# Optimization experiments

Hardware: AMD Instinct MI355X
Metric: run time of the kernel (lower is better)

Reference implementation:

```python
import jax, jax.numpy as jnp
import numpy as np

DIMS = [64, 128, 192, 256]   # Matryoshka sub-dims (init arg `dims`)
TEMPERATURE = 1.0
NEG_INF = float('-inf')
EPS = 1e-12  # F.normalize eps


def setup_inputs() -> dict:
    key = jax.random.key(0)
    k1, k2 = jax.random.split(key)
    B, K, D = 2048, 4096, 256
    reps_q = jax.random.normal(k1, (B, D), dtype=jnp.float32)
    reps_d = jax.random.normal(k2, (K, D), dtype=jnp.float32)
    return {"reps_q": reps_q, "reps_d": reps_d}


def _l2_normalize(x):
    n = jnp.linalg.norm(x, axis=1, keepdims=True)
    return x / jnp.maximum(n, EPS)


def _loss_for_dim(reps_q, reps_d, dim):
    q = _l2_normalize(reps_q[:, :dim])   # [B, dim]
    d = _l2_normalize(reps_d[:, :dim])   # [K, dim]
    B, K = q.shape[0], d.shape[0]

    qk = q @ d.T                         # [B, K]

    # check_pos_neg_pair_conflict (always True in the torch code)
    pos = d[:B]                          # positives are the first B keys
    sim = jax.lax.stop_gradient(pos @ d.T)               # [B, K], detached
    eye_bk = jnp.eye(B, K, dtype=bool)
    conflict = jnp.isclose(sim, 1.0, rtol=1e-5, atol=1e-5) & ~eye_bk
    qk = jnp.where(conflict, NEG_INF, qk)

    # use_all_pairs=True path: kq, qq, kk with -inf diagonals
    eye_bb = jnp.eye(B, dtype=bool)
    kq = jnp.where(eye_bb, NEG_INF, pos @ q.T)           # [B, B]
    qq = jnp.where(eye_bb, NEG_INF, q @ q.T)             # [B, B]
    kk = jnp.where(eye_bb, NEG_INF, pos @ pos.T)         # [B, B]

    scores = jnp.concatenate([qk, kq, qq, kk], axis=1)   # [B, K+3B]

    # check_false_neg: mask entries above diag(scores)+0.1 (thresholds detached)
    # diag(scores)[i] = scores[i, i] = qk[i, i] since B <= K
    thr = jax.lax.stop_gradient(jnp.diagonal(qk))[:, None] + 0.1
    scores = jnp.where(scores > thr, NEG_INF, scores)

    # cross-entropy with labels = arange(B)
    logp = jax.nn.log_softmax(scores / TEMPERATURE, axis=1)
    idx = jnp.arange(B)
    return -jnp.mean(logp[idx, idx])


def reference(reps_q, reps_d):
    loss = 0.0
    for dim in DIMS:
        loss = loss + _loss_for_dim(reps_q, reps_d, dim)
    return loss / len(DIMS)
```

## Files before the change

kernel.cpp:

```cpp
#include <hip/hip_runtime.h>

#define B_N 2048
#define K_N 4096
#define D_N 256
#define GRID_SCORE 3072
#define LOG2E 1.44269504f

typedef unsigned short u16;
typedef unsigned int u32;
typedef short short8 __attribute__((ext_vector_type(8)));
typedef float f32x4 __attribute__((ext_vector_type(4)));

__device__ __forceinline__ u16 f2bf(float x) {
    union { float f; u32 u; } v; v.f = x;
    u32 u = v.u;
    u32 lsb = (u >> 16) & 1u;
    u += 0x7fffu + lsb;
    return (u16)(u >> 16);
}
__device__ __forceinline__ float bits2f(u32 u) {
    union { u32 u; float f; } v; v.u = u; return v.f;
}

__global__ __launch_bounds__(256) void prep_kernel(
    const float* __restrict__ qsrc, const float* __restrict__ dsrc,
    u16* __restrict__ qb, u16* __restrict__ db,
    float* __restrict__ invnq, float* __restrict__ invnd, float* __restrict__ diag,
    float* __restrict__ rowsum, u32* __restrict__ doneCnt)
{
    if (blockIdx.x < 32) rowsum[blockIdx.x * 256 + threadIdx.x] = 0.f;
    if (blockIdx.x == 32 && threadIdx.x == 0)
        __hip_atomic_store(doneCnt, 0u, __ATOMIC_RELAXED, __HIP_MEMORY_SCOPE_AGENT);

    const int wave = threadIdx.x >> 6;
    const int lane = threadIdx.x & 63;
    const int row  = blockIdx.x * 4 + wave;

    if (row < B_N) {
        const int i = row;
        float4 qv = *(const float4*)(qsrc + i * D_N + lane * 4);
        float4 dv = *(const float4*)(dsrc + i * D_N + lane * 4);
        ushort4 qs; qs.x = f2bf(qv.x); qs.y = f2bf(qv.y); qs.z = f2bf(qv.z); qs.w = f2bf(qv.w);
        *(ushort4*)(qb + i * D_N + lane * 4) = qs;
        float sqq = qv.x*qv.x + qv.y*qv.y + qv.z*qv.z + qv.w*qv.w;
        float sdd = dv.x*dv.x + dv.y*dv.y + dv.z*dv.z + dv.w*dv.w;
        float sqd = qv.x*dv.x + qv.y*dv.y + qv.z*dv.z + qv.w*dv.w;
        #pragma unroll
        for (int m = 1; m < 16; m <<= 1) {
            sqq += __shfl_xor(sqq, m);
            sdd += __shfl_xor(sdd, m);
            sqd += __shfl_xor(sqd, m);
        }
        float gq0 = __shfl(sqq, 0),  gq1 = __shfl(sqq, 16), gq2 = __shfl(sqq, 32), gq3 = __shfl(sqq, 48);
        float gd0 = __shfl(sdd, 0),  gd1 = __shfl(sdd, 16), gd2 = __shfl(sdd, 32), gd3 = __shfl(sdd, 48);
        float gp0 = __shfl(sqd, 0),  gp1 = __shfl(sqd, 16), gp2 = __shfl(sqd, 32), gp3 = __shfl(sqd, 48);
        if (lane < 4) {
            float pq = gq0, pd = gd0, pp = gp0;
            if (lane >= 1) { pq += gq1; pd += gd1; pp += gp1; }
            if (lane >= 2) { pq += gq2; pd += gd2; pp += gp2; }
            if (lane >= 3) { pq += gq3; pd += gd3; pp += gp3; }
            float inq = 1.0f / fmaxf(sqrtf(pq), 1e-12f);
            float ind = 1.0f / fmaxf(sqrtf(pd), 1e-12f);
            invnq[i * 4 + lane] = inq;
            diag[i * 4 + lane]  = pp * inq * ind;
        }
    } else {
        const int j = row - B_N;
        float4 dv = *(const float4*)(dsrc + j * D_N + lane * 4);
        ushort4 ds; ds.x = f2bf(dv.x); ds.y = f2bf(dv.y); ds.z = f2bf(dv.z); ds.w = f2bf(dv.w);
        *(ushort4*)(db + j * D_N + lane * 4) = ds;
        float sdd = dv.x*dv.x + dv.y*dv.y + dv.z*dv.z + dv.w*dv.w;
        #pragma unroll
        for (int m = 1; m < 16; m <<= 1) sdd += __shfl_xor(sdd, m);
        float gd0 = __shfl(sdd, 0), gd1 = __shfl(sdd, 16), gd2 = __shfl(sdd, 32), gd3 = __shfl(sdd, 48);
        if (lane < 4) {
            float pd = gd0;
            if (lane >= 1) pd += gd1;
            if (lane >= 2) pd += gd2;
            if (lane >= 3) pd += gd3;
            invnd[j * 4 + lane] = 1.0f / fmaxf(sqrtf(pd), 1e-12f);
        }
    }
}

template<int RGN, bool EYE>
__device__ __forceinline__ void epi_seg(
    const f32x4* accq, const f32x4* accd,
    const float* ldsInvAq, const float* ldsInvAd, const float* ldsThr,
    const float* ldsInvB, float* ldsAcc,
    int s, int wrow, int quad, int lane15)
{
    const int myr = wrow + quad * 4;
    f32x4 ivAq = *(const f32x4*)(ldsInvAq + s * 64 + myr);
    f32x4 ivAd = *(const f32x4*)(ldsInvAd + s * 64 + myr);
    f32x4 thrv = *(const f32x4*)(ldsThr   + s * 64 + myr);
    float rsd[4] = {0.f, 0.f, 0.f, 0.f};
    #pragma unroll
    for (int ct = 0; ct < 4; ++ct) {
        const float ivB = ldsInvB[s * 64 + ct * 16 + lane15];
        const int jloc = ct * 16 + lane15;
        #pragma unroll
        for (int r = 0; r < 4; ++r) {
            const float thr = thrv[r];
            const float sq = accq[ct][r] * (ivAq[r] * ivB);
            const float sd = accd[ct][r] * (ivAd[r] * ivB);
            const bool eye = EYE && ((myr + r) == jloc);
            float add = 0.f;
            if (RGN <= 1) {
                bool conflict = (fabsf(sd - LOG2E) <= 2e-5f * LOG2E);
                if (EYE) conflict = conflict && !eye;
                if (!conflict && sq <= thr) add += exp2f(sq);
                if (RGN == 0) {
                    bool okk = (sd <= thr);
                    if (EYE) okk = okk && !eye;
                    if (okk) add += exp2f(sd);
                }
            } else {
                bool o1 = (sd <= thr), o2 = (sq <= thr);
                if (EYE) { o1 = o1 && !eye; o2 = o2 && !eye; }
                if (o1) add += exp2f(sd);
                if (o2) add += exp2f(sq);
            }
            rsd[r] += add;
        }
    }
    #pragma unroll
    for (int r = 0; r < 4; ++r) {
        float v = rsd[r];
        v += __shfl_xor(v, 1);
        v += __shfl_xor(v, 2);
        v += __shfl_xor(v, 4);
        v += __shfl_xor(v, 8);
        if (lane15 == 0)
            ldsAcc[(myr + r) * 4 + s] += v;
    }
}

#define LSB 264
__global__ __launch_bounds__(256, 4) void score_kernel(
    const u16* __restrict__ qb, const u16* __restrict__ db,
    const float* __restrict__ invnq, const float* __restrict__ invnd,
    const float* __restrict__ diag, float* __restrict__ rowsum,
    u32* __restrict__ doneCnt, u32* __restrict__ out)
{
    __shared__ u16   ldsB[64 * LSB];
    __shared__ float ldsInvAq[4 * 64];
    __shared__ float ldsInvAd[4 * 64];
    __shared__ float ldsThr[4 * 64];
    __shared__ float ldsInvB[4 * 64];
    __shared__ float ldsAcc[256];
    __shared__ u32   ldsLast;

    const int cb = blockIdx.x % 96;
    const int rb = blockIdx.x / 96;
    const int IR = rb * 64;
    const int JC = cb * 64;
    const bool isR3 = (cb >= 64);
    const bool isR1 = (cb < 32);
    const u16*  bsrc     = isR3 ? qb : db;
    const float* invBsrc = isR3 ? invnq : invnd;
    const int JB = isR3 ? (JC - K_N) : JC;
    const int sel = isR1 ? ((cb == rb) ? 1 : 0)
                  : (!isR3 ? 2 : (((cb - 64) == rb) ? 4 : 3));

    const int tid    = threadIdx.x;
    const int lane   = tid & 63;
    const int lane15 = lane & 15;
    const int quad   = lane >> 4;
    const int wrow   = (tid >> 6) * 16;

    {
        const int row = tid >> 2, s = tid & 3;
        ldsInvAq[s * 64 + row] = invnq[(IR + row) * 4 + s] * LOG2E;
        ldsInvAd[s * 64 + row] = invnd[(IR + row) * 4 + s] * LOG2E;
        ldsThr[s * 64 + row]   = (diag[(IR + row) * 4 + s] + 0.1f) * LOG2E;
        ldsInvB[s * 64 + row]  = invBsrc[(JB + row) * 4 + s];
        ldsAcc[tid] = 0.f;
    }

    #pragma unroll
    for (int c = 0; c < 8; ++c) {
        int idx = tid + c * 256;
        int row = idx >> 5;
        int ch  = idx & 31;
        uint4 v = *(const uint4*)(bsrc + (JB + row) * D_N + ch * 8);
        *(uint4*)(ldsB + row * LSB + ch * 8) = v;
    }

    const u16* qrowp = qb + (IR + wrow + lane15) * D_N + quad * 8;
    const u16* drowp = db + (IR + wrow + lane15) * D_N + quad * 8;

    short8 aq0 = *(const short8*)(qrowp);
    short8 aq1 = *(const short8*)(qrowp + 32);
    short8 ad0 = *(const short8*)(drowp);
    short8 ad1 = *(const short8*)(drowp + 32);

    __syncthreads();

    f32x4 accq[4], accd[4];
    #pragma unroll
    for (int ct = 0; ct < 4; ++ct) {
        accq[ct] = (f32x4){0.f, 0.f, 0.f, 0.f};
        accd[ct] = (f32x4){0.f, 0.f, 0.f, 0.f};
    }

    #pragma clang loop unroll(disable)
    for (int s = 0; s < 4; ++s) {
        const int sn = ((s + 1) & 3) * 64;
        short8 nq0 = *(const short8*)(qrowp + sn);
        short8 nq1 = *(const short8*)(qrowp + sn + 32);
        short8 nd0 = *(const short8*)(drowp + sn);
        short8 nd1 = *(const short8*)(drowp + sn + 32);

        #pragma unroll
        for (int ct = 0; ct < 4; ++ct) {
            short8 b0 = *(const short8*)(ldsB + (ct * 16 + lane15) * LSB + s * 64 + quad * 8);
            accq[ct] = __builtin_amdgcn_mfma_f32_16x16x32_bf16(aq0, b0, accq[ct], 0, 0, 0);
            accd[ct] = __builtin_amdgcn_mfma_f32_16x16x32_bf16(ad0, b0, accd[ct], 0, 0, 0);
        }
        #pragma unroll
        for (int ct = 0; ct < 4; ++ct) {
            short8 b1 = *(const short8*)(ldsB + (ct * 16 + lane15) * LSB + s * 64 + 32 + quad * 8);
            accq[ct] = __builtin_amdgcn_mfma_f32_16x16x32_bf16(aq1, b1, accq[ct], 0, 0, 0);
            accd[ct] = __builtin_amdgcn_mfma_f32_16x16x32_bf16(ad1, b1, accd[ct], 0, 0, 0);
        }
        if (sel == 0)      epi_seg<0,false>(accq, accd, ldsInvAq, ldsInvAd, ldsThr, ldsInvB, ldsAcc, s, wrow, quad, lane15);
        else if (sel == 1) epi_seg<0,true >(accq, accd, ldsInvAq, ldsInvAd, ldsThr, ldsInvB, ldsAcc, s, wrow, quad, lane15);
        else if (sel == 2) epi_seg<1,false>(accq, accd, ldsInvAq, ldsInvAd, ldsThr, ldsInvB, ldsAcc, s, wrow, quad, lane15);
        else if (sel == 3) epi_seg<2,false>(accq, accd, ldsInvAq, ldsInvAd, ldsThr, ldsInvB, ldsAcc, s, wrow, quad, lane15);
        else               epi_seg<2,true >(accq, accd, ldsInvAq, ldsInvAd, ldsThr, ldsInvB, ldsAcc, s, wrow, quad, lane15);

        aq0 = nq0; aq1 = nq1; ad0 = nd0; ad1 = nd1;
    }
    __syncthreads();

    atomicAdd(&rowsum[IR * 4 + tid], ldsAcc[tid]);
    __syncthreads();
    if (tid == 0) {
        u32 tk = __hip_atomic_fetch_add(doneCnt, 1u, __ATOMIC_RELAXED,
                                        __HIP_MEMORY_SCOPE_AGENT);
        ldsLast = (tk == (GRID_SCORE - 1)) ? 1u : 0u;
    }
    __syncthreads();

    if (ldsLast) {
        float acc = 0.f;
        #pragma unroll 8
        for (int c = 0; c < 32; ++c) {
            int idx = tid + c * 256;
            float rsv = __hip_atomic_load(&rowsum[idx], __ATOMIC_RELAXED,
                                          __HIP_MEMORY_SCOPE_AGENT);
            acc += logf(rsv) - diag[idx];
        }
        ldsAcc[tid] = acc;
        __syncthreads();
        #pragma unroll
        for (int off = 128; off > 0; off >>= 1) {
            if (tid < off) ldsAcc[tid] += ldsAcc[tid + off];
            __syncthreads();
        }
        if (tid == 0) {
            float L = ldsAcc[0] * (1.0f / (B_N * 4.0f));
            u16 h = f2bf(L);
            union { float f; u32 u; } b; b.f = L;
            u32 c0 = (b.u & 0xFFFF0000u) | (u32)h;
            u32 c1 = c0 + 0x10000u;
            u32 c2 = c0 - 0x10000u;
            float e0 = fabsf(bits2f(c0) - L);
            float e1 = fabsf(bits2f(c1) - L);
            float e2 = fabsf(bits2f(c2) - L);
            u32 best = c0; float be = e0;
            if (e1 < be) { best = c1; be = e1; }
            if (e2 < be) { best = c2; }
            out[0] = best;
        }
    }
}

extern "C" void kernel_launch(void* const* d_in, const int* in_sizes, int n_in,
                              void* d_out, int out_size, void* d_ws, size_t ws_size,
                              hipStream_t stream) {
    (void)in_sizes; (void)n_in; (void)out_size; (void)ws_size;
    const float* qsrc = (const float*)d_in[0];
    const float* dsrc = (const float*)d_in[1];
    char* ws = (char*)d_ws;
    u16*   qb      = (u16*)ws;
    u16*   db      = (u16*)(ws + 1048576);
    float* invnq   = (float*)(ws + 3145728);
    float* invnd   = (float*)(ws + 3178496);
    float* diag    = (float*)(ws + 3244032);
    float* rowsum  = (float*)(ws + 3276800);
    u32*   doneCnt = (u32*)(ws + 3309568);

    prep_kernel<<<1536, 256, 0, stream>>>(qsrc, dsrc, qb, db, invnq, invnd, diag,
                                          rowsum, doneCnt);
    score_kernel<<<GRID_SCORE, 256, 0, stream>>>(qb, db, invnq, invnd, diag, rowsum,
                                                 doneCnt, (u32*)d_out);
}
```

Measured before the change: 112.5 us.

## Exploit transpose symmetry of score blocks to skip redundant tile computations

The kq block is the transpose of the leading qk block, and qq is symmetric. Tiles are therefore restructured into four modes: qk+kk tiles that also add column contributions for kq, plain qk tiles, diagonal qq tiles, and upper-triangular qq tiles that add both row and column sums. This cuts the grid from 3072 to 2576 blocks and removes one MFMA stream from the q-only tiles. In exchange it adds LDS atomics for the column partials, extra global atomics into rowsum, and a small serial loop per block to decode the triangular index.

New measurement: 117.0 us. +4.0%, slower.

```diff
diff --git a/kernel.cpp b/kernel.cpp
--- a/kernel.cpp
+++ b/kernel.cpp
@@ -3,7 +3,7 @@
 #define B_N 2048
 #define K_N 4096
 #define D_N 256
-#define GRID_SCORE 3072
+#define GRID_SCORE 2576
 #define LOG2E 1.44269504f
 
 typedef unsigned short u16;
@@ -83,11 +83,11 @@
     }
 }
 
-template<int RGN, bool EYE>
-__device__ __forceinline__ void epi_seg(
+template<bool KK, bool EYE>
+__device__ __forceinline__ void epi2(
     const f32x4* accq, const f32x4* accd,
     const float* ldsInvAq, const float* ldsInvAd, const float* ldsThr,
-    const float* ldsInvB, float* ldsAcc,
+    const float* ldsInvB, const float* ldsThrB, float* ldsAcc, float* ldsAccCol,
     int s, int wrow, int quad, int lane15)
 {
     const int myr = wrow + quad * 4;
@@ -97,31 +97,79 @@
     float rsd[4] = {0.f, 0.f, 0.f, 0.f};
     #pragma unroll
     for (int ct = 0; ct < 4; ++ct) {
-        const float ivB = ldsInvB[s * 64 + ct * 16 + lane15];
         const int jloc = ct * 16 + lane15;
+        const float ivB  = ldsInvB[s * 64 + jloc];
+        const float thrB = KK ? ldsThrB[s * 64 + jloc] : 0.f;
+        float colp = 0.f;
         #pragma unroll
         for (int r = 0; r < 4; ++r) {
-            const float thr = thrv[r];
             const float sq = accq[ct][r] * (ivAq[r] * ivB);
             const float sd = accd[ct][r] * (ivAd[r] * ivB);
             const bool eye = EYE && ((myr + r) == jloc);
-            float add = 0.f;
-            if (RGN <= 1) {
-                bool conflict = (fabsf(sd - LOG2E) <= 2e-5f * LOG2E);
-                if (EYE) conflict = conflict && !eye;
-                if (!conflict && sq <= thr) add += exp2f(sq);
-                if (RGN == 0) {
-                    bool okk = (sd <= thr);
-                    if (EYE) okk = okk && !eye;
-                    if (okk) add += exp2f(sd);
-                }
+            bool conflict = (fabsf(sd - LOG2E) <= 2e-5f * LOG2E);
+            if (EYE) conflict = conflict && !eye;
+            const float eq = exp2f(sq);
+            if (!conflict && sq <= thrv[r]) rsd[r] += eq;
+            if (KK) {
+                bool okk = (sd <= thrv[r]);
+                if (EYE) okk = okk && !eye;
+                if (okk) rsd[r] += exp2f(sd);
+                bool okq = (sq <= thrB);
+                if (EYE) okq = okq && !eye;
+                if (okq) colp += eq;
+            }
+        }
+        if (KK) {
+            colp += __shfl_xor(colp, 16);
+            colp += __shfl_xor(colp, 32);
+            if (quad == 0) atomicAdd(&ldsAccCol[jloc * 4 + s], colp);
+        }
+    }
+    #pragma unroll
+    for (int r = 0; r < 4; ++r) {
+        float v = rsd[r];
+        v += __shfl_xor(v, 1);
+        v += __shfl_xor(v, 2);
+        v += __shfl_xor(v, 4);
+        v += __shfl_xor(v, 8);
+        if (lane15 == 0)
+            ldsAcc[(myr + r) * 4 + s] += v;
+    }
+}
+
+template<bool DUAL>
+__device__ __forceinline__ void epiQ(
+    const f32x4* accq,
+    const float* ldsInvAq, const float* ldsThr,
+    const float* ldsInvB, const float* ldsThrB, float* ldsAcc, float* ldsAccCol,
+    int s, int wrow, int quad, int lane15)
+{
+    const int myr = wrow + quad * 4;
+    f32x4 ivAq = *(const f32x4*)(ldsInvAq + s * 64 + myr);
+    f32x4 thrv = *(const f32x4*)(ldsThr   + s * 64 + myr);
+    float rsd[4] = {0.f, 0.f, 0.f, 0.f};
+    #pragma unroll
+    for (int ct = 0; ct < 4; ++ct) {
+        const int jloc = ct * 16 + lane15;
+        const float ivB  = ldsInvB[s * 64 + jloc];
+        const float thrB = DUAL ? ldsThrB[s * 64 + jloc] : 0.f;
+        float colp = 0.f;
+        #pragma unroll
+        for (int r = 0; r < 4; ++r) {
+            const float sq = accq[ct][r] * (ivAq[r] * ivB);
+            const float e = exp2f(sq);
+            if (!DUAL) {
+                const bool eye = ((myr + r) == jloc);
+                if (!eye && sq <= thrv[r]) rsd[r] += e;
             } else {
-                bool o1 = (sd <= thr), o2 = (sq <= thr);
-                if (EYE) { o1 = o1 && !eye; o2 = o2 && !eye; }
-                if (o1) add += exp2f(sd);
-                if (o2) add += exp2f(sq);
-            }
-            rsd[r] += add;
+                if (sq <= thrv[r]) rsd[r] += e;
+                if (sq <= thrB)    colp  += e;
+            }
+        }
+        if (DUAL) {
+            colp += __shfl_xor(colp, 16);
+            colp += __shfl_xor(colp, 32);
+            if (quad == 0) atomicAdd(&ldsAccCol[jloc * 4 + s], colp);
         }
     }
     #pragma unroll
@@ -148,20 +196,27 @@
     __shared__ float ldsInvAd[4 * 64];
     __shared__ float ldsThr[4 * 64];
     __shared__ float ldsInvB[4 * 64];
+    __shared__ float ldsThrB[4 * 64];
     __shared__ float ldsAcc[256];
-    __shared__ u32   ldsLast;
-
-    const int cb = blockIdx.x % 96;
-    const int rb = blockIdx.x / 96;
+    __shared__ float ldsAccCol[256];
+
+    const int bid = blockIdx.x;
+    int rb, cbl, mode;
+    if (bid < 1024)      { mode = 0; rb = bid >> 5; cbl = bid & 31; }
+    else if (bid < 2048) { mode = 1; int b = bid - 1024; rb = b >> 5; cbl = b & 31; }
+    else if (bid < 2080) { mode = 2; rb = bid - 2048; cbl = rb; }
+    else {
+        mode = 3; int k = bid - 2080; int a = 0;
+        while (k >= 31 - a) { k -= 31 - a; ++a; }
+        rb = a; cbl = a + 1 + k;
+    }
+    const bool qpl  = (mode >= 2);
+    const bool col  = (mode == 0 || mode == 3);
+    const bool eyeB = (mode == 0 && rb == cbl);
     const int IR = rb * 64;
-    const int JC = cb * 64;
-    const bool isR3 = (cb >= 64);
-    const bool isR1 = (cb < 32);
-    const u16*  bsrc     = isR3 ? qb : db;
-    const float* invBsrc = isR3 ? invnq : invnd;
-    const int JB = isR3 ? (JC - K_N) : JC;
-    const int sel = isR1 ? ((cb == rb) ? 1 : 0)
-                  : (!isR3 ? 2 : (((cb - 64) == rb) ? 4 : 3));
+    const int JB = (mode == 1) ? (B_N + cbl * 64) : (cbl * 64);
+    const u16*  bsrc     = qpl ? qb : db;
+    const float* invBsrc = qpl ? invnq : invnd;
 
     const int tid    = threadIdx.x;
     const int lane   = tid & 63;
@@ -175,7 +230,9 @@
         ldsInvAd[s * 64 + row] = invnd[(IR + row) * 4 + s] * LOG2E;
         ldsThr[s * 64 + row]   = (diag[(IR + row) * 4 + s] + 0.1f) * LOG2E;
         ldsInvB[s * 64 + row]  = invBsrc[(JB + row) * 4 + s];
+        ldsThrB[s * 64 + row]  = col ? (diag[(JB + row) * 4 + s] + 0.1f) * LOG2E : 0.f;
         ldsAcc[tid] = 0.f;
+        ldsAccCol[tid] = 0.f;
     }
 
     #pragma unroll
@@ -190,60 +247,87 @@
     const u16* qrowp = qb + (IR + wrow + lane15) * D_N + quad * 8;
     const u16* drowp = db + (IR + wrow + lane15) * D_N + quad * 8;
 
-    short8 aq0 = *(const short8*)(qrowp);
-    short8 aq1 = *(const short8*)(qrowp + 32);
-    short8 ad0 = *(const short8*)(drowp);
-    short8 ad1 = *(const short8*)(drowp + 32);
-
+    if (!qpl) {
+        short8 aq0 = *(const short8*)(qrowp);
+        short8 aq1 = *(const short8*)(qrowp + 32);
+        short8 ad0 = *(const short8*)(drowp);
+        short8 ad1 = *(const short8*)(drowp + 32);
+        __syncthreads();
+
+        f32x4 accq[4], accd[4];
+        #pragma unroll
+        for (int ct = 0; ct < 4; ++ct) {
+            accq[ct] = (f32x4){0.f, 0.f, 0.f, 0.f};
+            accd[ct] = (f32x4){0.f, 0.f, 0.f, 0.f};
+        }
+        #pragma clang loop unroll(disable)
+        for (int s = 0; s < 4; ++s) {
+            const int sn = ((s + 1) & 3) * 64;
+            short8 nq0 = *(const short8*)(qrowp + sn);
+            short8 nq1 = *(const short8*)(qrowp + sn + 32);
+            short8 nd0 = *(const short8*)(drowp + sn);
+            short8 nd1 = *(const short8*)(drowp + sn + 32);
+            #pragma unroll
+            for (int ct = 0; ct < 4; ++ct) {
+                short8 b0 = *(const short8*)(ldsB + (ct * 16 + lane15) * LSB + s * 64 + quad * 8);
+                accq[ct] = __builtin_amdgcn_mfma_f32_16x16x32_bf16(aq0, b0, accq[ct], 0, 0, 0);
+                accd[ct] = __builtin_amdgcn_mfma_f32_16x16x32_bf16(ad0, b0, accd[ct], 0, 0, 0);
+            }
+            #pragma unroll
+            for (int ct = 0; ct < 4; ++ct) {
+                short8 b1 = *(const short8*)(ldsB + (ct * 16 + lane15) * LSB + s * 64 + 32 + quad * 8);
+                accq[ct] = __builtin_amdgcn_mfma_f32_16x16x32_bf16(aq1, b1, accq[ct], 0, 0, 0);
+                accd[ct] = __builtin_amdgcn_mfma_f32_16x16x32_bf16(ad1, b1, accd[ct], 0, 0, 0);
+            }
+            if (mode == 0) {
+                if (eyeB) epi2<true,true >(accq, accd, ldsInvAq, ldsInvAd, ldsThr, ldsInvB, ldsThrB, ldsAcc, ldsAccCol, s, wrow, quad, lane15);
+                else      epi2<true,false>(accq, accd, ldsInvAq, ldsInvAd, ldsThr, ldsInvB, ldsThrB, ldsAcc, ldsAccCol, s, wrow, quad, lane15);
+            } else {
+                epi2<false,false>(accq, accd, ldsInvAq, ldsInvAd, ldsThr, ldsInvB, ldsThrB, ldsAcc, ldsAccCol, s, wrow, quad, lane15);
+            }
+            aq0 = nq0; aq1 = nq1; ad0 = nd0; ad1 = nd1;
+        }
+    } else {
+        short8 aq0 = *(const short8*)(qrowp);
+        short8 aq1 = *(const short8*)(qrowp + 32);
+        __syncthreads();
+
+        f32x4 accq[4];
+        #pragma unroll
+        for (int ct = 0; ct < 4; ++ct) accq[ct] = (f32x4){0.f, 0.f, 0.f, 0.f};
+        #pragma clang loop unroll(disable)
+        for (int s = 0; s < 4; ++s) {
+            const int sn = ((s + 1) & 3) * 64;
+            short8 nq0 = *(const short8*)(qrowp + sn);
+            short8 nq1 = *(const short8*)(qrowp + sn + 32);
+            #pragma unroll
+            for (int ct = 0; ct < 4; ++ct) {
+                short8 b0 = *(const short8*)(ldsB + (ct * 16 + lane15) * LSB + s * 64 + quad * 8);
+                accq[ct] = __builtin_amdgcn_mfma_f32_16x16x32_bf16(aq0, b0, accq[ct], 0, 0, 0);
+            }
+            #pragma unroll
+            for (int ct = 0; ct < 4; ++ct) {
+                short8 b1 = *(const short8*)(ldsB + (ct * 16 + lane15) * LSB + s * 64 + 32 + quad * 8);
+                accq[ct] = __builtin_amdgcn_mfma_f32_16x16x32_bf16(aq1, b1, accq[ct], 0, 0, 0);
+            }
+            if (mode == 2) epiQ<false>(accq, ldsInvAq, ldsThr, ldsInvB, ldsThrB, ldsAcc, ldsAccCol, s, wrow, quad, lane15);
+            else           epiQ<true >(accq, ldsInvAq, ldsThr, ldsInvB, ldsThrB, ldsAcc, ldsAccCol, s, wrow, quad, lane15);
+            aq0 = nq0; aq1 = nq1;
+        }
+    }
     __syncthreads();
 
-    f32x4 accq[4], accd[4];
-    #pragma unroll
-    for (int ct = 0; ct < 4; ++ct) {
-        accq[ct] = (f32x4){0.f, 0.f, 0.f, 0.f};
-        accd[ct] = (f32x4){0.f, 0.f, 0.f, 0.f};
-    }
-
-    #pragma clang loop unroll(disable)
-    for (int s = 0; s < 4; ++s) {
-        const int sn = ((s + 1) & 3) * 64;
-        short8 nq0 = *(const short8*)(qrowp + sn);
-        short8 nq1 = *(const short8*)(qrowp + sn + 32);
-        short8 nd0 = *(const short8*)(drowp + sn);
-        short8 nd1 = *(const short8*)(drowp + sn + 32);
-
-        #pragma unroll
-        for (int ct = 0; ct < 4; ++ct) {
-            short8 b0 = *(const short8*)(ldsB + (ct * 16 + lane15) * LSB + s * 64 + quad * 8);
-            accq[ct] = __builtin_amdgcn_mfma_f32_16x16x32_bf16(aq0, b0, accq[ct], 0, 0, 0);
-            accd[ct] = __builtin_amdgcn_mfma_f32_16x16x32_bf16(ad0, b0, accd[ct], 0, 0, 0);
-        }
-        #pragma unroll
-        for (int ct = 0; ct < 4; ++ct) {
-            short8 b1 = *(const short8*)(ldsB + (ct * 16 + lane15) * LSB + s * 64 + 32 + quad * 8);
-            accq[ct] = __builtin_amdgcn_mfma_f32_16x16x32_bf16(aq1, b1, accq[ct], 0, 0, 0);
-            accd[ct] = __builtin_amdgcn_mfma_f32_16x16x32_bf16(ad1, b1, accd[ct], 0, 0, 0);
-        }
-        if (sel == 0)      epi_seg<0,false>(accq, accd, ldsInvAq, ldsInvAd, ldsThr, ldsInvB, ldsAcc, s, wrow, quad, lane15);
-        else if (sel == 1) epi_seg<0,true >(accq, accd, ldsInvAq, ldsInvAd, ldsThr, ldsInvB, ldsAcc, s, wrow, quad, lane15);
-        else if (sel == 2) epi_seg<1,false>(accq, accd, ldsInvAq, ldsInvAd, ldsThr, ldsInvB, ldsAcc, s, wrow, quad, lane15);
-        else if (sel == 3) epi_seg<2,false>(accq, accd, ldsInvAq, ldsInvAd, ldsThr, ldsInvB, ldsAcc, s, wrow, quad, lane15);
-        else               epi_seg<2,true >(accq, accd, ldsInvAq, ldsInvAd, ldsThr, ldsInvB, ldsAcc, s, wrow, quad, lane15);
-
-        aq0 = nq0; aq1 = nq1; ad0 = nd0; ad1 = nd1;
-    }
-    __syncthreads();
-
     atomicAdd(&rowsum[IR * 4 + tid], ldsAcc[tid]);
+    if (col) atomicAdd(&rowsum[JB * 4 + tid], ldsAccCol[tid]);
     __syncthreads();
     if (tid == 0) {
         u32 tk = __hip_atomic_fetch_add(doneCnt, 1u, __ATOMIC_RELAXED,
                                         __HIP_MEMORY_SCOPE_AGENT);
-        ldsLast = (tk == (GRID_SCORE - 1)) ? 1u : 0u;
+        ldsAccCol[0] = (tk == (GRID_SCORE - 1)) ? 1.f : 0.f;
     }
     __syncthreads();
 
-    if (ldsLast) {
+    if (ldsAccCol[0] != 0.f) {
         float acc = 0.f;
         #pragma unroll 8
         for (int c = 0; c < 32; ++c) {
```
